# Performance work log

Measured on AMD Instinct MI355X. Metric: run time of the kernel, lower is better.

The kernel has to match this reference:

```python
import jax, jax.numpy as jnp
import numpy as np

G = 1024        # graphs in batch
NPG = 64        # nodes per graph
EPG = 256       # edges per graph
N = G * NPG     # 65536 total nodes
E = G * EPG     # 262144 total edges
IN_CH = 768
CH = 128
RATIO = 0.5
K = int(RATIO * EPG)  # edges reserved as 'causal' per graph


def setup_inputs() -> dict:
    key = jax.random.key(0)
    ks = jax.random.split(key, 10)
    w = lambda k, shape, fan: (jax.random.normal(k, shape, jnp.float32) / np.float32(np.sqrt(fan)))
    x = jax.random.normal(ks[0], (N, IN_CH), jnp.float32)
    # per-graph random edges, offset into the global node index space
    ei = jax.random.randint(ks[1], (2, G, EPG), 0, NPG)
    edge_index = (ei + (jnp.arange(G) * NPG)[None, :, None]).reshape(2, -1).astype(jnp.int32)
    edge_attr = jax.random.uniform(ks[2], (E,), jnp.float32)  # positive edge weights
    batch = jnp.repeat(jnp.arange(G, dtype=jnp.int32), NPG)
    return dict(
        x=x, edge_index=edge_index, edge_attr=edge_attr, batch=batch,
        W1=w(ks[3], (IN_CH, CH), IN_CH), V1=w(ks[4], (IN_CH, CH), IN_CH), b1=jnp.zeros((CH,), jnp.float32),
        W2=w(ks[5], (CH, CH), CH),       V2=w(ks[6], (CH, CH), CH),       b2=jnp.zeros((CH,), jnp.float32),
        mw1=w(ks[7], (2 * CH, 4 * CH), 2 * CH), mb1=jnp.zeros((4 * CH,), jnp.float32),
        mw2=w(ks[8], (4 * CH, 1), 4 * CH),      mb2=jnp.zeros((1,), jnp.float32),
    )


def reference(x, edge_index, edge_attr, batch, W1, V1, b1, W2, V2, b2, mw1, mb1, mw2, mb2):
    row, col = edge_index[0], edge_index[1]
    ew = edge_attr.reshape(-1)

    # gcn_norm (symmetric, no self loops), as used inside ARMAConv
    deg = jnp.zeros((N,), x.dtype).at[col].add(ew)
    dis = jnp.where(deg > 0, jax.lax.rsqrt(jnp.where(deg > 0, deg, 1.0)), 0.0)
    norm = dis[row] * ew * dis[col]  # [E]

    def arma(h, W, V, b):
        # ARMAConv, num_stacks=1, num_layers=1: ReLU(A_hat (h W) + h V + b)
        m = h @ W                                            # [N, C]
        agg = jnp.zeros((N, W.shape[1]), h.dtype).at[col].add(norm[:, None] * m[row])
        return jax.nn.relu(agg + h @ V + b)

    x1 = jax.nn.relu(arma(x, W1, V1, b1))  # outer F.relu (idempotent after internal ReLU)
    x2 = arma(x1, W2, V2, b2)              # [N, CH]

    # edge-gather MLP -> scalar score per edge
    edge_rep = jnp.concatenate([x2[row], x2[col]], axis=-1)          # [E, 2C]
    pred_edge_weight = (jax.nn.relu(edge_rep @ mw1 + mb1) @ mw2 + mb2).reshape(-1)  # [E]

    # per-graph top-k split (batched replacement of the numpy argpartition loop)
    wg = pred_edge_weight.reshape(G, EPG)
    order = jnp.argsort(-wg, axis=1)                                  # descending
    base = (jnp.arange(G) * EPG)[:, None]
    cid = (base + order[:, :K]).reshape(-1)   # causal (reserved) edge ids
    did = (base + order[:, K:]).reshape(-1)   # conf (dropped) edge ids

    causal = (x2, edge_index[:, cid], edge_attr[cid], pred_edge_weight[cid], batch)
    conf = (x2, edge_index[:, did], edge_attr[did], -pred_edge_weight[did], batch)
    return (*causal, *conf, pred_edge_weight)
```

## Files before the change

kernel.cpp:

```cpp
#include <hip/hip_runtime.h>
#include <hip/hip_bf16.h>
#include <stdint.h>

#define G_    1024
#define NPG   64
#define EPG   256
#define N_    (G_*NPG)
#define E_    (G_*EPG)
#define IN_CH 768
#define CH    128
#define KSEL  128
#define HID   512

#define NCH  (N_*CH)
#define GK   (G_*KSEL)
#define OFF0 0
#define OFF1 (OFF0 + NCH)
#define OFF2 (OFF1 + 2*GK)
#define OFF3 (OFF2 + GK)
#define OFF4 (OFF3 + GK)
#define OFF5 (OFF4 + N_)
#define OFF6 (OFF5 + NCH)
#define OFF7 (OFF6 + 2*GK)
#define OFF8 (OFF7 + GK)
#define OFF9 (OFF8 + GK)
#define OFF10 (OFF9 + N_)

typedef unsigned short u16;
typedef unsigned int   u32;
typedef __attribute__((ext_vector_type(8))) short bf16x8;
typedef __attribute__((ext_vector_type(4))) float f32x4;

__device__ __forceinline__ u16 f2bf(float x) {
    union { float f; u32 u; } v; v.f = x;
    u32 r = v.u + 0x7fffu + ((v.u >> 16) & 1u);
    return (u16)(r >> 16);
}
__device__ __forceinline__ float bf2f(u32 h) {
    union { u32 u; float f; } v; v.u = h << 16; return v.f;
}
__device__ __forceinline__ u16 bfc(float x) {
    __hip_bfloat16 h = __float2bfloat16(x);
    return *reinterpret_cast<u16*>(&h);
}

__global__ void k_deg(const int* __restrict__ ei, const float* __restrict__ ea,
                      float* __restrict__ deg) {
    int e = blockIdx.x * 256 + threadIdx.x;
    if (e < E_) atomicAdd(&deg[ei[E_ + e]], ea[e]);
}

__global__ void k_norm(const int* __restrict__ ei, const float* __restrict__ ea,
                       const float* __restrict__ deg, float* __restrict__ norm) {
    int e = blockIdx.x * 256 + threadIdx.x;
    if (e >= E_) return;
    float dr = deg[ei[e]], dc = deg[ei[E_ + e]];
    float fr = dr > 0.f ? 1.0f / sqrtf(dr) : 0.f;
    float fc = dc > 0.f ? 1.0f / sqrtf(dc) : 0.f;
    norm[e] = fr * ea[e] * fc;
}

__global__ void k_concat(const float* __restrict__ W1, const float* __restrict__ V1,
                         const float* __restrict__ W2, const float* __restrict__ V2,
                         const float* __restrict__ mw1,
                         u16* __restrict__ WV1t, u16* __restrict__ WV2t,
                         u16* __restrict__ Mwt) {
    int i = blockIdx.x * 256 + threadIdx.x;
    if (i < 256 * IN_CH) {
        int c = i / IN_CH, r = i - c * IN_CH;
        WV1t[i] = f2bf(c < CH ? W1[r*CH + c] : V1[r*CH + (c - CH)]);
    }
    if (i < 256 * CH) {
        int c = i >> 7, r = i & 127;
        WV2t[i] = f2bf(c < CH ? W2[r*CH + c] : V2[r*CH + (c - CH)]);
    }
    if (i < 1024 * CH) {
        int c = i >> 7, r = i & 127;
        Mwt[i] = f2bf(c < HID ? mw1[r*HID + c] : mw1[(CH + r)*HID + (c - HID)]);
    }
}

__global__ __launch_bounds__(256) void k_gemm1(const float* __restrict__ Ap,
        const u16* __restrict__ Bt, u16* __restrict__ Cp) {
    __shared__ float As[2][128 * 32];
    const int t = threadIdx.x;
    const int lane = t & 63, w = t >> 6;
    const int wr = (w >> 1) << 6, wc = (w & 1) << 6;
    const size_t bm = (size_t)blockIdx.x * 128;
    const size_t bn = (size_t)blockIdx.y * 128;
    const int r16 = lane & 15, kq = lane >> 4;

    int cid[4], grow[4], gcol[4];
    #pragma unroll
    for (int i = 0; i < 4; ++i) {
        int c = i * 256 + t;
        cid[i] = c;
        int row = c >> 3, sl = c & 7;
        grow[i] = row;
        gcol[i] = (sl ^ (row & 7)) * 4;
    }

    f32x4 acc[4][4];
    #pragma unroll
    for (int m = 0; m < 4; ++m)
        #pragma unroll
        for (int n = 0; n < 4; ++n)
            acc[m][n] = (f32x4){0.f, 0.f, 0.f, 0.f};

    #define STAGE(buf, k0)                                                      \
        do {                                                                    \
            _Pragma("unroll")                                                   \
            for (int i = 0; i < 4; ++i) {                                       \
                const float* src = Ap + (bm + grow[i]) * (size_t)IN_CH + (k0) + gcol[i]; \
                __builtin_amdgcn_global_load_lds(                               \
                    (const __attribute__((address_space(1))) void*)src,         \
                    (__attribute__((address_space(3))) void*)&As[buf][cid[i] * 4], \
                    16, 0, 0);                                                  \
            }                                                                   \
        } while (0)

    #define LOADB(bv, k0)                                                       \
        do {                                                                    \
            _Pragma("unroll")                                                   \
            for (int n = 0; n < 4; ++n)                                         \
                bv[n] = *(const bf16x8*)(Bt + (bn + wc + n * 16 + r16) * (size_t)IN_CH + (k0) + kq * 8); \
        } while (0)

    STAGE(0, 0);
    bf16x8 bc[4];
    LOADB(bc, 0);
    __syncthreads();

    const int nk = IN_CH / 32;
    int buf = 0;
    for (int ki = 0; ki < nk; ++ki) {
        bf16x8 bnx[4];
        if (ki + 1 < nk) {
            STAGE(buf ^ 1, (ki + 1) * 32);
            LOADB(bnx, (ki + 1) * 32);
        }
        bf16x8 a[4];
        #pragma unroll
        for (int m = 0; m < 4; ++m) {
            int row = wr + m * 16 + r16;
            int xr = row & 7;
            const float* base = &As[buf][row * 32];
            float4 q0 = *(const float4*)(base + (((2 * kq)     ^ xr) * 4));
            float4 q1 = *(const float4*)(base + (((2 * kq + 1) ^ xr) * 4));
            union { bf16x8 v; u16 s[8]; } pk;
            pk.s[0] = bfc(q0.x); pk.s[1] = bfc(q0.y); pk.s[2] = bfc(q0.z); pk.s[3] = bfc(q0.w);
            pk.s[4] = bfc(q1.x); pk.s[5] = bfc(q1.y); pk.s[6] = bfc(q1.z); pk.s[7] = bfc(q1.w);
            a[m] = pk.v;
        }
        #pragma unroll
        for (int m = 0; m < 4; ++m)
            #pragma unroll
            for (int n = 0; n < 4; ++n)
                acc[m][n] = __builtin_amdgcn_mfma_f32_16x16x32_bf16(a[m], bc[n], acc[m][n], 0, 0, 0);
        if (ki + 1 < nk) {
            #pragma unroll
            for (int n = 0; n < 4; ++n) bc[n] = bnx[n];
        }
        __syncthreads();
        buf ^= 1;
    }
    #undef STAGE
    #undef LOADB

    #pragma unroll
    for (int m = 0; m < 4; ++m)
        #pragma unroll
        for (int j = 0; j < 4; ++j) {
            size_t row = bm + wr + m * 16 + kq * 4 + j;
            #pragma unroll
            for (int n = 0; n < 4; ++n) {
                size_t col = bn + wc + n * 16 + r16;
                Cp[row * 256 + col] = f2bf(acc[m][n][j]);
            }
        }
}

__global__ __launch_bounds__(512, 4) void k_graph(const u16* __restrict__ B1b,
        const u16* __restrict__ WV2t, const u16* __restrict__ Mwt,
        const int* __restrict__ ei, const float* __restrict__ norm,
        const float* __restrict__ b1, const float* __restrict__ b2,
        const float* __restrict__ mb1, const float* __restrict__ mw2,
        const float* __restrict__ mb2, const float* __restrict__ ea,
        float* __restrict__ out) {
    __shared__ char Lds[70912];
    float* A_s   = (float*)(Lds + 0);
    float* key   = (float*)(Lds + 0);
    int*   idx   = (int*)(Lds + 1024);
    u16*   x1s   = (u16*)(Lds + 16640);
    u16*   x2s   = (u16*)(Lds + 16640);
    u16*   Ms    = (u16*)(Lds + 34048);
    u16*   MVs   = (u16*)(Lds + 34048);
    u16*   PQc   = (u16*)(Lds + 34048);
    float* mw2s  = (float*)(Lds + 68864);

    const int g = blockIdx.x, t = threadIdx.x;
    const int lane = t & 63, w = t >> 6;
    const int r16 = lane & 15, kq = lane >> 4;
    const size_t nbase = (size_t)g * 64;
    union bfr { bf16x8 v; u16 s[8]; };

    if (t < 128) *(float4*)&mw2s[t * 4] = *(const float4*)&mw2[t * 4];
    for (int i = t; i < 64 * 65; i += 512) A_s[i] = 0.f;
    for (int i = t; i < 64 * 32; i += 512) {
        int row = i >> 5, c4 = (i & 31) << 2;
        *(uint2*)&Ms[row * 136 + c4] = *(const uint2*)(B1b + (nbase + row) * 256 + c4);
    }
    int er = 0, ec = 0; float env = 0.f;
    if (t < 256) { int e = g * 256 + t; er = ei[e] & 63; ec = ei[E_ + e] & 63; env = norm[e]; }
    __syncthreads();
    if (t < 256) atomicAdd(&A_s[er * 65 + ec], env);
    __syncthreads();

    {
        const int n0 = w * 16;
        f32x4 acc[4];
        #pragma unroll
        for (int mt = 0; mt < 4; ++mt) acc[mt] = (f32x4){0.f, 0.f, 0.f, 0.f};
        #pragma unroll
        for (int ks = 0; ks < 2; ++ks) {
            bfr a[4], b;
            #pragma unroll
            for (int mt = 0; mt < 4; ++mt)
                #pragma unroll
                for (int i = 0; i < 8; ++i)
                    a[mt].s[i] = f2bf(A_s[(ks*32 + kq*8 + i) * 65 + mt*16 + r16]);
            #pragma unroll
            for (int i = 0; i < 8; ++i)
                b.s[i] = Ms[(ks*32 + kq*8 + i) * 136 + n0 + r16];
            #pragma unroll
            for (int mt = 0; mt < 4; ++mt)
                acc[mt] = __builtin_amdgcn_mfma_f32_16x16x32_bf16(a[mt].v, b.v, acc[mt], 0, 0, 0);
        }
        const int ch = w * 16 + r16;
        __syncthreads();
        #pragma unroll
        for (int mt = 0; mt < 4; ++mt)
            #pragma unroll
            for (int j = 0; j < 4; ++j) {
                int c = mt * 16 + kq * 4 + j;
                float v = bf2f(B1b[(nbase + c) * 256 + 128 + ch]) + b1[ch];
                x1s[c * 136 + ch] = f2bf(fmaxf(acc[mt][j] + v, 0.f));
            }
    }
    __syncthreads();

    {
        const int wc2 = w * 32;
        f32x4 acc[4][2];
        #pragma unroll
        for (int mt = 0; mt < 4; ++mt)
            #pragma unroll
            for (int n = 0; n < 2; ++n) acc[mt][n] = (f32x4){0.f, 0.f, 0.f, 0.f};
        #pragma unroll
        for (int ks = 0; ks < 4; ++ks) {
            bf16x8 a[4], b[2];
            #pragma unroll
            for (int mt = 0; mt < 4; ++mt)
                a[mt] = *(const bf16x8*)&x1s[(mt*16 + r16) * 136 + ks*32 + kq*8];
            #pragma unroll
            for (int n = 0; n < 2; ++n)
                b[n] = *(const bf16x8*)(WV2t + (size_t)(wc2 + n*16 + r16) * 128 + ks*32 + kq*8);
            #pragma unroll
            for (int mt = 0; mt < 4; ++mt)
                #pragma unroll
                for (int n = 0; n < 2; ++n)
                    acc[mt][n] = __builtin_amdgcn_mfma_f32_16x16x32_bf16(a[mt], b[n], acc[mt][n], 0, 0, 0);
        }
        #pragma unroll
        for (int mt = 0; mt < 4; ++mt)
            #pragma unroll
            for (int j = 0; j < 4; ++j) {
                int row = mt * 16 + kq * 4 + j;
                #pragma unroll
                for (int n = 0; n < 2; ++n)
                    MVs[row * 272 + wc2 + n*16 + r16] = f2bf(acc[mt][n][j]);
            }
    }
    __syncthreads();

    {
        const int n0 = w * 16;
        f32x4 acc[4];
        #pragma unroll
        for (int mt = 0; mt < 4; ++mt) acc[mt] = (f32x4){0.f, 0.f, 0.f, 0.f};
        #pragma unroll
        for (int ks = 0; ks < 2; ++ks) {
            bfr a[4], b;
            #pragma unroll
            for (int mt = 0; mt < 4; ++mt)
                #pragma unroll
                for (int i = 0; i < 8; ++i)
                    a[mt].s[i] = f2bf(A_s[(ks*32 + kq*8 + i) * 65 + mt*16 + r16]);
            #pragma unroll
            for (int i = 0; i < 8; ++i)
                b.s[i] = MVs[(ks*32 + kq*8 + i) * 272 + n0 + r16];
            #pragma unroll
            for (int mt = 0; mt < 4; ++mt)
                acc[mt] = __builtin_amdgcn_mfma_f32_16x16x32_bf16(a[mt].v, b.v, acc[mt], 0, 0, 0);
        }
        const int ch = w * 16 + r16;
        #pragma unroll
        for (int mt = 0; mt < 4; ++mt)
            #pragma unroll
            for (int j = 0; j < 4; ++j) {
                int c = mt * 16 + kq * 4 + j;
                float v = bf2f(MVs[c * 272 + 128 + ch]) + b2[ch];
                float r = fmaxf(acc[mt][j] + v, 0.f);
                size_t node = nbase + c;
                out[OFF0 + node * 128 + ch] = r;
                out[OFF5 + node * 128 + ch] = r;
                x2s[c * 136 + ch] = f2bf(r);
            }
    }
    __syncthreads();

    const int le = lane & 31, jh = lane >> 5;
    const int eloc = w * 32 + le;
    const int e_g = g * 256 + eloc;
    const int er6 = ei[e_g] & 63, ec6 = ei[E_ + e_g] & 63;
    float esum = 0.f;
    #pragma unroll 1
    for (int h = 0; h < 4; ++h) {
        const int wc5 = w * 32;
        f32x4 acc[4][2];
        #pragma unroll
        for (int mt = 0; mt < 4; ++mt)
            #pragma unroll
            for (int n = 0; n < 2; ++n) acc[mt][n] = (f32x4){0.f, 0.f, 0.f, 0.f};
        #pragma unroll
        for (int ks = 0; ks < 4; ++ks) {
            bf16x8 a[4], b[2];
            #pragma unroll
            for (int mt = 0; mt < 4; ++mt)
                a[mt] = *(const bf16x8*)&x2s[(mt*16 + r16) * 136 + ks*32 + kq*8];
            #pragma unroll
            for (int n = 0; n < 2; ++n) {
                int colc = wc5 + n * 16 + r16;
                int mwrow = (colc < 128) ? (h * 128 + colc) : (512 + h * 128 + (colc - 128));
                b[n] = *(const bf16x8*)(Mwt + (size_t)mwrow * 128 + ks*32 + kq*8);
            }
            #pragma unroll
            for (int mt = 0; mt < 4; ++mt)
                #pragma unroll
                for (int n = 0; n < 2; ++n)
                    acc[mt][n] = __builtin_amdgcn_mfma_f32_16x16x32_bf16(a[mt], b[n], acc[mt][n], 0, 0, 0);
        }
        #pragma unroll
        for (int n = 0; n < 2; ++n) {
            int colc = wc5 + n * 16 + r16;
            float bias = (colc < 128) ? mb1[h * 128 + colc] : 0.f;
            #pragma unroll
            for (int mt = 0; mt < 4; ++mt)
                #pragma unroll
                for (int j = 0; j < 4; ++j) {
                    int row = mt * 16 + kq * 4 + j;
                    PQc[row * 260 + colc] = f2bf(acc[mt][n][j] + bias);
                }
        }
        __syncthreads();
        {
            const u16* pP = &PQc[er6 * 260 + jh * 64];
            const u16* pQ = &PQc[ec6 * 260 + 128 + jh * 64];
            const float* pW = &mw2s[h * 128 + jh * 64];
            #pragma unroll
            for (int it = 0; it < 8; ++it) {
                uint4 up = *(const uint4*)(pP + it * 8);
                uint4 uq = *(const uint4*)(pQ + it * 8);
                float4 w0 = *(const float4*)(pW + it * 8);
                float4 w1 = *(const float4*)(pW + it * 8 + 4);
                u32 pu[4] = {up.x, up.y, up.z, up.w};
                u32 qu[4] = {uq.x, uq.y, uq.z, uq.w};
                float ww[8] = {w0.x,w0.y,w0.z,w0.w,w1.x,w1.y,w1.z,w1.w};
                #pragma unroll
                for (int k = 0; k < 4; ++k) {
                    float p0 = bf2f(pu[k] & 0xffffu), p1 = bf2f(pu[k] >> 16);
                    float q0 = bf2f(qu[k] & 0xffffu), q1 = bf2f(qu[k] >> 16);
                    esum += fmaxf(p0 + q0, 0.f) * ww[2*k];
                    esum += fmaxf(p1 + q1, 0.f) * ww[2*k + 1];
                }
            }
        }
        __syncthreads();
    }
    {
        float s = esum + __shfl_xor(esum, 32, 64);
        if (lane < 32) {
            float pv = s + mb2[0];
            out[OFF10 + e_g] = pv;
            key[eloc] = pv;
            idx[eloc] = eloc;
        }
    }

    for (int k2 = 2; k2 <= 256; k2 <<= 1) {
        for (int j = k2 >> 1; j >= 1; j >>= 1) {
            __syncthreads();
            if (t < 256) {
                int ixj = t ^ j;
                if (ixj > t) {
                    float ka = key[t], kb = key[ixj];
                    int   ia = idx[t], ib = idx[ixj];
                    bool up = ((t & k2) == 0);
                    bool a_before_b = (ka > kb) || (ka == kb && ia < ib);
                    bool do_swap = up ? !a_before_b : a_before_b;
                    if (do_swap) { key[t] = kb; key[ixj] = ka; idx[t] = ib; idx[ixj] = ia; }
                }
            }
        }
    }
    __syncthreads();
    if (t < 256) {
        int el = idx[t];
        int eg = g * 256 + el;
        float pv = key[t];
        float r = (float)ei[eg];
        float c = (float)ei[E_ + eg];
        float av = ea[eg];
        if (t < KSEL) {
            int oo = g * KSEL + t;
            out[OFF1 + oo]      = r;
            out[OFF1 + GK + oo] = c;
            out[OFF2 + oo]      = av;
            out[OFF3 + oo]      = pv;
        } else {
            int oo = g * KSEL + (t - KSEL);
            out[OFF6 + oo]      = r;
            out[OFF6 + GK + oo] = c;
            out[OFF7 + oo]      = av;
            out[OFF8 + oo]      = -pv;
        }
    }
    if (t < 64) {
        out[OFF4 + nbase + t] = (float)g;
        out[OFF9 + nbase + t] = (float)g;
    }
}

extern "C" void kernel_launch(void* const* d_in, const int* in_sizes, int n_in,
                              void* d_out, int out_size, void* d_ws, size_t ws_size,
                              hipStream_t stream) {
    const float* x     = (const float*)d_in[0];
    const int*   ei    = (const int*)  d_in[1];
    const float* ea    = (const float*)d_in[2];
    const float* W1    = (const float*)d_in[4];
    const float* V1    = (const float*)d_in[5];
    const float* b1    = (const float*)d_in[6];
    const float* W2    = (const float*)d_in[7];
    const float* V2    = (const float*)d_in[8];
    const float* b2    = (const float*)d_in[9];
    const float* mw1   = (const float*)d_in[10];
    const float* mb1   = (const float*)d_in[11];
    const float* mw2   = (const float*)d_in[12];
    const float* mb2   = (const float*)d_in[13];
    float* out = (float*)d_out;

    char* ws = (char*)d_ws;
    size_t o = 0;
    float* deg  = (float*)(ws + o); o += (size_t)N_ * 4;
    float* norm = (float*)(ws + o); o += (size_t)E_ * 4;
    u16* WV1t   = (u16*)(ws + o);   o += (size_t)256 * IN_CH * 2;
    u16* WV2t   = (u16*)(ws + o);   o += (size_t)256 * CH * 2;
    u16* Mwt    = (u16*)(ws + o);   o += (size_t)1024 * CH * 2;
    u16* B1b    = (u16*)(ws + o);   o += (size_t)N_ * 256 * 2;

    hipMemsetAsync(deg, 0, (size_t)N_ * 4, stream);
    k_deg <<<E_/256, 256, 0, stream>>>(ei, ea, deg);
    k_norm<<<E_/256, 256, 0, stream>>>(ei, ea, deg, norm);
    k_concat<<<768, 256, 0, stream>>>(W1, V1, W2, V2, mw1, WV1t, WV2t, Mwt);

    dim3 g1(N_/128, 2);
    k_gemm1<<<g1, 256, 0, stream>>>(x, WV1t, B1b);

    k_graph<<<G_, 512, 0, stream>>>(B1b, WV2t, Mwt, ei, norm, b1, b2,
                                    mb1, mw2, mb2, ea, out);
}
```

Measured before the change: 232.6 us.

## Fuse degree/norm into per-graph kernel and replace bitonic sort with rank counting

Degree accumulation and symmetric normalization move into the per-graph kernel using shared-memory atomics, which removes the memset and two global kernels and the norm round-trip through global memory. This is valid because each graph's edges stay inside its own node block. The bitonic sort with many barriers is replaced by each thread counting how many keys beat its own, giving its rank directly. Edge data stays in registers, so the post-sort gathers are gone, at the cost of O(256) reads from LDS per thread.

```diff
diff --git a/kernel.cpp b/kernel.cpp
--- a/kernel.cpp
+++ b/kernel.cpp
@@ -44,22 +44,6 @@
     return *reinterpret_cast<u16*>(&h);
 }
 
-__global__ void k_deg(const int* __restrict__ ei, const float* __restrict__ ea,
-                      float* __restrict__ deg) {
-    int e = blockIdx.x * 256 + threadIdx.x;
-    if (e < E_) atomicAdd(&deg[ei[E_ + e]], ea[e]);
-}
-
-__global__ void k_norm(const int* __restrict__ ei, const float* __restrict__ ea,
-                       const float* __restrict__ deg, float* __restrict__ norm) {
-    int e = blockIdx.x * 256 + threadIdx.x;
-    if (e >= E_) return;
-    float dr = deg[ei[e]], dc = deg[ei[E_ + e]];
-    float fr = dr > 0.f ? 1.0f / sqrtf(dr) : 0.f;
-    float fc = dc > 0.f ? 1.0f / sqrtf(dc) : 0.f;
-    norm[e] = fr * ea[e] * fc;
-}
-
 __global__ void k_concat(const float* __restrict__ W1, const float* __restrict__ V1,
                          const float* __restrict__ W2, const float* __restrict__ V2,
                          const float* __restrict__ mw1,
@@ -182,21 +166,21 @@
 
 __global__ __launch_bounds__(512, 4) void k_graph(const u16* __restrict__ B1b,
         const u16* __restrict__ WV2t, const u16* __restrict__ Mwt,
-        const int* __restrict__ ei, const float* __restrict__ norm,
+        const int* __restrict__ ei,
         const float* __restrict__ b1, const float* __restrict__ b2,
         const float* __restrict__ mb1, const float* __restrict__ mw2,
         const float* __restrict__ mb2, const float* __restrict__ ea,
         float* __restrict__ out) {
-    __shared__ char Lds[70912];
+    __shared__ char Lds[71168];
     float* A_s   = (float*)(Lds + 0);
     float* key   = (float*)(Lds + 0);
-    int*   idx   = (int*)(Lds + 1024);
     u16*   x1s   = (u16*)(Lds + 16640);
     u16*   x2s   = (u16*)(Lds + 16640);
     u16*   Ms    = (u16*)(Lds + 34048);
     u16*   MVs   = (u16*)(Lds + 34048);
     u16*   PQc   = (u16*)(Lds + 34048);
     float* mw2s  = (float*)(Lds + 68864);
+    float* deg_s = (float*)(Lds + 70912);
 
     const int g = blockIdx.x, t = threadIdx.x;
     const int lane = t & 63, w = t >> 6;
@@ -206,14 +190,27 @@
 
     if (t < 128) *(float4*)&mw2s[t * 4] = *(const float4*)&mw2[t * 4];
     for (int i = t; i < 64 * 65; i += 512) A_s[i] = 0.f;
+    if (t < 64) deg_s[t] = 0.f;
     for (int i = t; i < 64 * 32; i += 512) {
         int row = i >> 5, c4 = (i & 31) << 2;
         *(uint2*)&Ms[row * 136 + c4] = *(const uint2*)(B1b + (nbase + row) * 256 + c4);
     }
-    int er = 0, ec = 0; float env = 0.f;
-    if (t < 256) { int e = g * 256 + t; er = ei[e] & 63; ec = ei[E_ + e] & 63; env = norm[e]; }
-    __syncthreads();
-    if (t < 256) atomicAdd(&A_s[er * 65 + ec], env);
+    int rfull = 0, cfull = 0, er = 0, ec = 0; float eav = 0.f;
+    if (t < 256) {
+        int e = g * 256 + t;
+        rfull = ei[e]; cfull = ei[E_ + e];
+        er = rfull & 63; ec = cfull & 63;
+        eav = ea[e];
+    }
+    __syncthreads();
+    if (t < 256) atomicAdd(&deg_s[ec], eav);
+    __syncthreads();
+    if (t < 256) {
+        float dr = deg_s[er], dc = deg_s[ec];
+        float fr = dr > 0.f ? 1.0f / sqrtf(dr) : 0.f;
+        float fc = dc > 0.f ? 1.0f / sqrtf(dc) : 0.f;
+        atomicAdd(&A_s[er * 65 + ec], fr * eav * fc);
+    }
     __syncthreads();
 
     {
@@ -393,46 +390,37 @@
             float pv = s + mb2[0];
             out[OFF10 + e_g] = pv;
             key[eloc] = pv;
-            idx[eloc] = eloc;
-        }
-    }
-
-    for (int k2 = 2; k2 <= 256; k2 <<= 1) {
-        for (int j = k2 >> 1; j >= 1; j >>= 1) {
-            __syncthreads();
-            if (t < 256) {
-                int ixj = t ^ j;
-                if (ixj > t) {
-                    float ka = key[t], kb = key[ixj];
-                    int   ia = idx[t], ib = idx[ixj];
-                    bool up = ((t & k2) == 0);
-                    bool a_before_b = (ka > kb) || (ka == kb && ia < ib);
-                    bool do_swap = up ? !a_before_b : a_before_b;
-                    if (do_swap) { key[t] = kb; key[ixj] = ka; idx[t] = ib; idx[ixj] = ia; }
-                }
-            }
-        }
-    }
-    __syncthreads();
+        }
+    }
+    __syncthreads();
+
     if (t < 256) {
-        int el = idx[t];
-        int eg = g * 256 + el;
-        float pv = key[t];
-        float r = (float)ei[eg];
-        float c = (float)ei[E_ + eg];
-        float av = ea[eg];
-        if (t < KSEL) {
-            int oo = g * KSEL + t;
+        float ki = key[t];
+        int rank = 0;
+        const float4* k4 = (const float4*)key;
+        #pragma unroll 4
+        for (int j4 = 0; j4 < 64; ++j4) {
+            float4 kv = k4[j4];
+            int j = j4 * 4;
+            rank += (kv.x > ki) || (kv.x == ki && (j + 0) < t);
+            rank += (kv.y > ki) || (kv.y == ki && (j + 1) < t);
+            rank += (kv.z > ki) || (kv.z == ki && (j + 2) < t);
+            rank += (kv.w > ki) || (kv.w == ki && (j + 3) < t);
+        }
+        float r = (float)rfull;
+        float c = (float)cfull;
+        if (rank < KSEL) {
+            int oo = g * KSEL + rank;
             out[OFF1 + oo]      = r;
             out[OFF1 + GK + oo] = c;
-            out[OFF2 + oo]      = av;
-            out[OFF3 + oo]      = pv;
+            out[OFF2 + oo]      = eav;
+            out[OFF3 + oo]      = ki;
         } else {
-            int oo = g * KSEL + (t - KSEL);
+            int oo = g * KSEL + (rank - KSEL);
             out[OFF6 + oo]      = r;
             out[OFF6 + GK + oo] = c;
-            out[OFF7 + oo]      = av;
-            out[OFF8 + oo]      = -pv;
+            out[OFF7 + oo]      = eav;
+            out[OFF8 + oo]      = -ki;
         }
     }
     if (t < 64) {
@@ -461,21 +449,16 @@
 
     char* ws = (char*)d_ws;
     size_t o = 0;
-    float* deg  = (float*)(ws + o); o += (size_t)N_ * 4;
-    float* norm = (float*)(ws + o); o += (size_t)E_ * 4;
     u16* WV1t   = (u16*)(ws + o);   o += (size_t)256 * IN_CH * 2;
     u16* WV2t   = (u16*)(ws + o);   o += (size_t)256 * CH * 2;
     u16* Mwt    = (u16*)(ws + o);   o += (size_t)1024 * CH * 2;
     u16* B1b    = (u16*)(ws + o);   o += (size_t)N_ * 256 * 2;
 
-    hipMemsetAsync(deg, 0, (size_t)N_ * 4, stream);
-    k_deg <<<E_/256, 256, 0, stream>>>(ei, ea, deg);
-    k_norm<<<E_/256, 256, 0, stream>>>(ei, ea, deg, norm);
     k_concat<<<768, 256, 0, stream>>>(W1, V1, W2, V2, mw1, WV1t, WV2t, Mwt);
 
     dim3 g1(N_/128, 2);
     k_gemm1<<<g1, 256, 0, stream>>>(x, WV1t, B1b);
 
-    k_graph<<<G_, 512, 0, stream>>>(B1b, WV2t, Mwt, ei, norm, b1, b2,
+    k_graph<<<G_, 512, 0, stream>>>(B1b, WV2t, Mwt, ei, b1, b2,
                                     mb1, mw2, mb2, ea, out);
 }
```

Measured after the change: 215.3 us. 1.08x faster.
